# Kernel optimization log

Hardware: AMD Instinct MI355X
Metric: run time of the kernel (lower is better)

Reference implementation:

```python
import jax, jax.numpy as jnp
import numpy as np

B, L, DIN, DQ, DS, DP = 16, 2048, 1024, 128, 64, 32

def _lin(k, din, dout):
    k1, k2 = jax.random.split(k)
    s = 1.0 / np.sqrt(din)
    W = jax.random.uniform(k1, (din, dout), jnp.float32, -s, s)
    b = jax.random.uniform(k2, (dout,), jnp.float32, -s, s)
    return W, b

def setup_inputs() -> dict:
    key = jax.random.key(0)
    ks = jax.random.split(key, 13)
    Wq, bq = _lin(ks[0], DIN, DQ)
    Wk, bk = _lin(ks[1], DIN, DQ)
    Wv, bv = _lin(ks[2], DIN, DQ)
    W1, b1 = _lin(ks[3], DS + DP, 128)
    W2, b2 = _lin(ks[4], 128, DQ)
    Wqc, bqc = _lin(ks[5], DQ, DQ)
    Wkc, bkc = _lin(ks[6], DQ, DQ)
    return dict(
        query=jax.random.normal(ks[7], (B, L, DIN), jnp.float32),
        key=jax.random.normal(ks[8], (B, L, DIN), jnp.float32),
        value=jax.random.normal(ks[9], (B, L, DIN), jnp.float32),
        sf=jax.random.normal(ks[10], (B, DS), jnp.float32),
        pos=jax.random.normal(ks[11], (L, DP), jnp.float32),
        Wq=Wq, bq=bq, Wk=Wk, bk=bk, Wv=Wv, bv=bv,
        W1=W1, b1=b1, W2=W2, b2=b2,
        Wqc=Wqc, bqc=bqc, Wkc=Wkc, bkc=bkc,
    )

def reference(query, key, value, sf, pos,
              Wq, bq, Wk, bk, Wv, bv,
              W1, b1, W2, b2, Wqc, bqc, Wkc, bkc):
    b, l, _ = query.shape
    q = query @ Wq + bq            # [b, l, dq]
    k = key @ Wk + bk              # [b, l, dq]
    v = value @ Wv + bv            # [b, l, dq]
    # CPE bias branch (pos is not None)
    sf_exp = jnp.broadcast_to(sf[:, None, :], (b, l, sf.shape[1]))
    pos_exp = jnp.broadcast_to(pos[None, :, :], (b, l, pos.shape[1]))
    cpe = jnp.concatenate([sf_exp, pos_exp], axis=2)         # [b, l, ds+32]
    cpe = jax.nn.relu(cpe @ W1 + b1) @ W2 + b2               # [b, l, dq]
    qc = cpe @ Wqc + bqc
    kc = cpe @ Wkc + bkc
    bias = jnp.einsum('bld,bmd->blm', qc, kc)                # [b, l, l]
    # add_mode == 0: post-softmax additive bias
    scale = jnp.sqrt(jnp.asarray(q.shape[-1], q.dtype))
    scores = jnp.einsum('bld,bmd->blm', q, k) / scale
    attn = jax.nn.softmax(scores, axis=-1) + bias
    out = jnp.einsum('blm,bmd->bld', attn, v)
    # L1 diff-norm regularizer over bias (use_cls=False)
    norm3 = (jnp.sum(jnp.abs(bias[:, 1:, :] - bias[:, :-1, :])) +
             jnp.sum(jnp.abs(bias[:, :, 1:] - bias[:, :, :-1])))
    return out, norm3
```

## Files before the change

### kernel.cpp

```cpp
#include <hip/hip_runtime.h>
#include <hip/hip_bf16.h>

typedef __attribute__((ext_vector_type(8))) short short8;
typedef __attribute__((ext_vector_type(4))) short short4x;
typedef __attribute__((ext_vector_type(4))) float floatx4;

#define MFMA16(a,b,c) __builtin_amdgcn_mfma_f32_16x16x32_bf16((a),(b),(c),0,0,0)

__device__ __forceinline__ unsigned short f2bf(float f) {
  unsigned int x = __float_as_uint(f);
  return (unsigned short)((x + 0x7fffu + ((x >> 16) & 1u)) >> 16);
}
__device__ __forceinline__ float bf2f(unsigned short s) {
  return __uint_as_float(((unsigned int)s) << 16);
}
__device__ __forceinline__ unsigned short f2bf_cvt(float f) {
  unsigned int r;
  asm("v_cvt_pk_bf16_f32 %0, %1, %1" : "=v"(r) : "v"(f));
  return (unsigned short)r;
}
__device__ __forceinline__ short8 pack8(float4 f0, float4 f1) {
  union { unsigned int u[4]; short8 s; } r;
  asm("v_cvt_pk_bf16_f32 %0, %1, %2" : "=v"(r.u[0]) : "v"(f0.x), "v"(f0.y));
  asm("v_cvt_pk_bf16_f32 %0, %1, %2" : "=v"(r.u[1]) : "v"(f0.z), "v"(f0.w));
  asm("v_cvt_pk_bf16_f32 %0, %1, %2" : "=v"(r.u[2]) : "v"(f1.x), "v"(f1.y));
  asm("v_cvt_pk_bf16_f32 %0, %1, %2" : "=v"(r.u[3]) : "v"(f1.z), "v"(f1.w));
  return r.s;
}

typedef const __attribute__((address_space(1))) void* gas_ptr;
typedef __attribute__((address_space(3))) void* las_ptr;
__device__ __forceinline__ void gload_lds16(const void* g, void* s) {
  __builtin_amdgcn_global_load_lds((gas_ptr)g, (las_ptr)s, 16, 0, 0);
}

__global__ __launch_bounds__(256)
void prep_kernel(const float* __restrict__ Wq, const float* __restrict__ Wk,
                 const float* __restrict__ Wv, const float* __restrict__ W1,
                 const float* __restrict__ b1, const float* __restrict__ W2,
                 const float* __restrict__ b2, const float* __restrict__ Wqc,
                 const float* __restrict__ bqc, const float* __restrict__ Wkc,
                 const float* __restrict__ bkc, const float* __restrict__ sf,
                 const float* __restrict__ pos,
                 unsigned short* __restrict__ Wf, unsigned short* __restrict__ Ut,
                 float* __restrict__ cqck, float* __restrict__ Asf,
                 float* __restrict__ Ppos)
{
  int blk = blockIdx.x, t = threadIdx.x;
  if (blk < 24) {
    int mat = blk >> 3, cg = blk & 7;
    const float* W = (mat == 0) ? Wq : (mat == 1) ? Wk : Wv;
    int l = t & 63, jp = t >> 6;
    int col = cg * 16 + (l & 15);
    unsigned short* o = Wf + (size_t)mat * 131072 + (size_t)cg * 32 * 512 + l * 8 + jp * 2;
    for (int ks = 0; ks < 32; ++ks) {
      int k = ks * 32 + (l >> 4) * 8 + jp * 2;
      o[ks * 512 + 0] = f2bf(W[(size_t)k * 128 + col]);
      o[ks * 512 + 1] = f2bf(W[(size_t)(k + 1) * 128 + col]);
    }
  } else if (blk >= 384 && blk < 512) {
    int j = blk - 384;
    int k = t & 127;
    const float* Wc = (t < 128) ? Wqc : Wkc;
    float acc = 0.f;
    for (int h = 0; h < 128; ++h) acc += W2[k * 128 + h] * Wc[h * 128 + j];
    Ut[(size_t)((t < 128) ? j : 128 + j) * 128 + k] = f2bf(acc);
  } else if (blk == 512) {
    int j = t & 127;
    const float* Wc = (t < 128) ? Wqc : Wkc;
    const float* bc = (t < 128) ? bqc : bkc;
    float acc = bc[j];
    for (int k = 0; k < 128; ++k) acc += b2[k] * Wc[k * 128 + j];
    cqck[t] = acc;
  } else if (blk > 512 && blk < 529) {
    int b = blk - 513;
    if (t < 128) {
      float acc = 0.f;
      for (int i = 0; i < 64; ++i) acc += sf[b * 64 + i] * W1[i * 128 + t];
      Asf[b * 128 + t] = acc;
    }
  } else if (blk >= 529) {
    int l = blk - 529;
    if (t < 128) {
      float acc = b1[t];
      for (int i = 0; i < 32; ++i) acc += pos[l * 32 + i] * W1[(64 + i) * 128 + t];
      Ppos[l * 128 + t] = acc;
    }
  }
}

__global__ __launch_bounds__(256)
void proj_kernel(const float* __restrict__ X, const unsigned short* __restrict__ Wf,
                 const float* __restrict__ bias,
                 unsigned short* __restrict__ qo, unsigned short* __restrict__ ko,
                 unsigned short* __restrict__ vto, int which)
{
  __shared__ __align__(16) float X_lds[16 * 1028];

  int t = threadIdx.x, w = t >> 6, l = t & 63;
  int rowbase = blockIdx.x * 16;
  const int lrow = l & 15, hi = l >> 4;
  const float RS2 = 0.08838834764831845f * 1.4426950408889634f;

#pragma unroll
  for (int i = 0; i < 16; ++i) {
    int row = w * 4 + (i >> 2), seg = i & 3;
    gload_lds16(X + (size_t)(rowbase + row) * 1024 + seg * 256 + l * 4,
                (char*)X_lds + (size_t)row * 4112 + seg * 1024);
  }
  __syncthreads();

  const unsigned short* wp0 = Wf + (size_t)(w * 2) * 32 * 512 + l * 8;
  const unsigned short* wp1 = Wf + (size_t)(w * 2 + 1) * 32 * 512 + l * 8;
  const float* ap = &X_lds[lrow * 1028 + hi * 8];

  floatx4 acc0, acc1;
  acc0[0]=0.f; acc0[1]=0.f; acc0[2]=0.f; acc0[3]=0.f;
  acc1[0]=0.f; acc1[1]=0.f; acc1[2]=0.f; acc1[3]=0.f;

#pragma unroll 4
  for (int ks = 0; ks < 32; ++ks) {
    short8 b0 = *(const short8*)(wp0 + ks * 512);
    short8 b1 = *(const short8*)(wp1 + ks * 512);
    float4 f0 = *(const float4*)(ap + ks * 32);
    float4 f1 = *(const float4*)(ap + ks * 32 + 4);
    short8 a = pack8(f0, f1);
    acc0 = MFMA16(a, b0, acc0);
    acc1 = MFMA16(a, b1, acc1);
  }

#pragma unroll
  for (int nf = 0; nf < 2; ++nf) {
    int col = w * 32 + nf * 16 + lrow;
    float bb = bias[col];
    floatx4 av = (nf == 0) ? acc0 : acc1;
#pragma unroll
    for (int j = 0; j < 4; ++j) {
      int grow = rowbase + hi * 4 + j;
      float v = av[j] + bb;
      if (which == 0) qo[(size_t)grow * 128 + col] = f2bf(v * RS2);
      else if (which == 1) ko[(size_t)grow * 128 + col] = f2bf(v);
      else {
        int b = grow >> 11, li = grow & 2047;
        vto[((size_t)b * 128 + col) * 2048 + li] = f2bf(v);
      }
    }
  }
}

__global__ __launch_bounds__(256)
void qckc_kernel(const float* __restrict__ Asf, const float* __restrict__ Ppos,
                 const unsigned short* __restrict__ Ut, const float* __restrict__ cqck,
                 unsigned short* __restrict__ qc, unsigned short* __restrict__ kc)
{
  __shared__ __align__(16) unsigned short hid[64 * 136];
  int t = threadIdx.x, w = t >> 6, l = t & 63;
  int lbase = blockIdx.x * 64;
  int b = lbase >> 11;
  const int lrow = l & 15, lk = (l >> 4) * 8;
  {
    int r = t >> 2, seg = (t & 3) * 32;
    const float* pp = Ppos + (size_t)((lbase + r) & 2047) * 128 + seg;
    const float* aa = Asf + b * 128 + seg;
    unsigned short* dst = hid + r * 136 + seg;
#pragma unroll
    for (int c = 0; c < 32; c += 4) {
      float4 p4 = *(const float4*)(pp + c);
      float4 a4 = *(const float4*)(aa + c);
      dst[c + 0] = f2bf(fmaxf(p4.x + a4.x, 0.f));
      dst[c + 1] = f2bf(fmaxf(p4.y + a4.y, 0.f));
      dst[c + 2] = f2bf(fmaxf(p4.z + a4.z, 0.f));
      dst[c + 3] = f2bf(fmaxf(p4.w + a4.w, 0.f));
    }
  }
  __syncthreads();
  short8 a[4];
#pragma unroll
  for (int ks = 0; ks < 4; ++ks)
    a[ks] = *(const short8*)&hid[(w * 16 + lrow) * 136 + ks * 32 + lk];
  floatx4 acc[16];
#pragma unroll
  for (int nf = 0; nf < 16; ++nf) { acc[nf][0]=0.f; acc[nf][1]=0.f; acc[nf][2]=0.f; acc[nf][3]=0.f; }
#pragma unroll
  for (int nf = 0; nf < 16; ++nf)
#pragma unroll
    for (int ks = 0; ks < 4; ++ks) {
      short8 bfr = *(const short8*)(Ut + (size_t)(nf * 16 + lrow) * 128 + ks * 32 + lk);
      acc[nf] = MFMA16(a[ks], bfr, acc[nf]);
    }
#pragma unroll
  for (int nf = 0; nf < 16; ++nf) {
    int col = nf * 16 + lrow;
    float bb = cqck[col];
#pragma unroll
    for (int j = 0; j < 4; ++j) {
      int grow = lbase + w * 16 + (l >> 4) * 4 + j;
      float v = acc[nf][j] + bb;
      if (col < 128) qc[(size_t)grow * 128 + col] = f2bf(v);
      else kc[(size_t)grow * 128 + (col - 128)] = f2bf(v);
    }
  }
}

__global__ __launch_bounds__(256)
void m2_partial_kernel(const unsigned short* __restrict__ vt,
                       const unsigned short* __restrict__ kc,
                       float* __restrict__ M2p)
{
  __shared__ __align__(16) unsigned short kct[128 * 40];
  int ks = blockIdx.x, b = blockIdx.y;
  int t = threadIdx.x, w = t >> 6, l = t & 63;
  const int lrow = l & 15, lk = (l >> 4) * 8;
  floatx4 acc[2][8];
#pragma unroll
  for (int i = 0; i < 2; ++i)
#pragma unroll
    for (int j = 0; j < 8; ++j) { acc[i][j][0]=0.f; acc[i][j][1]=0.f; acc[i][j][2]=0.f; acc[i][j][3]=0.f; }
  for (int mc = 0; mc < 8; ++mc) {
    int mbase = ks * 256 + mc * 32;
    {
      int mm = t & 31, ib = (t >> 5) * 16;
      const unsigned short* src = kc + ((size_t)b * 2048 + mbase + mm) * 128 + ib;
#pragma unroll
      for (int ii = 0; ii < 16; ++ii) kct[(ib + ii) * 40 + mm] = src[ii];
    }
    __syncthreads();
#pragma unroll
    for (int mf = 0; mf < 2; ++mf) {
      int jrow = w * 32 + mf * 16 + lrow;
      short8 a = *(const short8*)(vt + ((size_t)b * 128 + jrow) * 2048 + mbase + lk);
#pragma unroll
      for (int nf = 0; nf < 8; ++nf) {
        short8 bfr = *(const short8*)&kct[(nf * 16 + lrow) * 40 + lk];
        acc[mf][nf] = MFMA16(a, bfr, acc[mf][nf]);
      }
    }
    __syncthreads();
  }
#pragma unroll
  for (int mf = 0; mf < 2; ++mf)
#pragma unroll
    for (int nf = 0; nf < 8; ++nf)
#pragma unroll
      for (int j = 0; j < 4; ++j) {
        int jr = w * 32 + mf * 16 + (l >> 4) * 4 + j;
        int ic = nf * 16 + lrow;
        M2p[(((size_t)ks * 16 + b) * 128 + jr) * 128 + ic] = acc[mf][nf][j];
      }
}

__global__ void m2_reduce_kernel(const float* __restrict__ M2p, float* __restrict__ M2t)
{
  int idx = blockIdx.x * 256 + threadIdx.x;
  float s = 0.f;
#pragma unroll
  for (int ksp = 0; ksp < 8; ++ksp) s += M2p[(size_t)ksp * 262144 + idx];
  M2t[idx] = s;
}

__global__ __launch_bounds__(256)
void attn_partial_kernel(const unsigned short* __restrict__ qbf,
                         const unsigned short* __restrict__ kbf,
                         const unsigned short* __restrict__ vt,
                         float* __restrict__ op, float* __restrict__ ms)
{
  __shared__ __align__(16) unsigned short K_lds[64 * 136];
  __shared__ __align__(16) unsigned short V_lds[128 * 72];
  __shared__ __align__(16) unsigned short P_lds[4 * 16 * 72];
  int t = threadIdx.x, w = t >> 6, l = t & 63;
  int lbase = blockIdx.x * 64, b = blockIdx.y, z = blockIdx.z;
  const int lrow = l & 15, lk = (l >> 4) * 8;

  size_t browq = (size_t)b * 2048 + lbase + w * 16 + lrow;
  short8 aq[4];
#pragma unroll
  for (int ks = 0; ks < 4; ++ks)
    aq[ks] = *(const short8*)(qbf + browq * 128 + ks * 32 + lk);

  float m_run[4] = {-1e30f, -1e30f, -1e30f, -1e30f};
  float s_run[4] = {0.f, 0.f, 0.f, 0.f};
  floatx4 o[8];
#pragma unroll
  for (int nf = 0; nf < 8; ++nf) { o[nf][0]=0.f; o[nf][1]=0.f; o[nf][2]=0.f; o[nf][3]=0.f; }

  int sr = t >> 2, sseg = (t & 3) * 32;
  int vr = t >> 1, vseg = (t & 1) * 32;

  const short8* ksrc0 = (const short8*)(kbf + ((size_t)b * 2048 + z * 1024 + sr) * 128 + sseg);
  const short8* vsrc0 = (const short8*)(vt + ((size_t)b * 128 + vr) * 2048 + z * 1024 + vseg);

  short8 kr[4], vrg[4];
#pragma unroll
  for (int i = 0; i < 4; ++i) { kr[i] = ksrc0[i]; vrg[i] = vsrc0[i]; }

  for (int kt = 0; kt < 16; ++kt) {
    {
      short8* dst = (short8*)&K_lds[sr * 136 + sseg];
      dst[0] = kr[0]; dst[1] = kr[1]; dst[2] = kr[2]; dst[3] = kr[3];
      short8* vdst = (short8*)&V_lds[vr * 72 + vseg];
      vdst[0] = vrg[0]; vdst[1] = vrg[1]; vdst[2] = vrg[2]; vdst[3] = vrg[3];
    }
    __syncthreads();
    if (kt < 15) {
      const short8* ks2 = ksrc0 + (size_t)(kt + 1) * 1024;
      const short8* vs2 = vsrc0 + (size_t)(kt + 1) * 8;
#pragma unroll
      for (int i = 0; i < 4; ++i) { kr[i] = ks2[i]; vrg[i] = vs2[i]; }
    }
    floatx4 s[4];
    __builtin_amdgcn_s_setprio(1);
#pragma unroll
    for (int cf = 0; cf < 4; ++cf) {
      floatx4 a4; a4[0]=0.f; a4[1]=0.f; a4[2]=0.f; a4[3]=0.f;
#pragma unroll
      for (int ks = 0; ks < 4; ++ks) {
        short8 bfr = *(const short8*)&K_lds[(cf * 16 + lrow) * 136 + ks * 32 + lk];
        a4 = MFMA16(aq[ks], bfr, a4);
      }
      s[cf] = a4;
    }
    __builtin_amdgcn_s_setprio(0);
    float tm[4];
#pragma unroll
    for (int j = 0; j < 4; ++j) {
      float m0 = fmaxf(fmaxf(s[0][j], s[1][j]), fmaxf(s[2][j], s[3][j]));
#pragma unroll
      for (int off = 1; off < 16; off <<= 1) m0 = fmaxf(m0, __shfl_xor(m0, off, 64));
      tm[j] = m0;
    }
    bool need = (tm[0] > m_run[0] + 8.f) | (tm[1] > m_run[1] + 8.f) |
                (tm[2] > m_run[2] + 8.f) | (tm[3] > m_run[3] + 8.f);
    if (__any(need)) {
      float fmul[4];
#pragma unroll
      for (int j = 0; j < 4; ++j) {
        float nm = fmaxf(m_run[j], tm[j]);
        fmul[j] = exp2f(m_run[j] - nm);
        m_run[j] = nm;
        s_run[j] *= fmul[j];
      }
#pragma unroll
      for (int nf = 0; nf < 8; ++nf)
#pragma unroll
        for (int j = 0; j < 4; ++j) o[nf][j] *= fmul[j];
    }
#pragma unroll
    for (int j = 0; j < 4; ++j) {
      float rs = 0.f;
#pragma unroll
      for (int cf = 0; cf < 4; ++cf) {
        float p = exp2f(s[cf][j] - m_run[j]);
        s[cf][j] = p;
        rs += p;
      }
#pragma unroll
      for (int off = 1; off < 16; off <<= 1) rs += __shfl_xor(rs, off, 64);
      s_run[j] += rs;
    }
    unsigned short* pw = P_lds + w * (16 * 72);
#pragma unroll
    for (int cf = 0; cf < 4; ++cf)
#pragma unroll
      for (int j = 0; j < 4; ++j)
        pw[((l >> 4) * 4 + j) * 72 + cf * 16 + lrow] = f2bf_cvt(s[cf][j]);
    __builtin_amdgcn_s_setprio(1);
#pragma unroll
    for (int kf = 0; kf < 2; ++kf) {
      short8 ap = *(const short8*)&pw[lrow * 72 + kf * 32 + lk];
#pragma unroll
      for (int nf = 0; nf < 8; ++nf) {
        short8 bv = *(const short8*)&V_lds[(nf * 16 + lrow) * 72 + kf * 32 + lk];
        o[nf] = MFMA16(ap, bv, o[nf]);
      }
    }
    __builtin_amdgcn_s_setprio(0);
    __syncthreads();
  }
  size_t obase = (size_t)(z * 16 + b) * 2048;
#pragma unroll
  for (int nf = 0; nf < 8; ++nf)
#pragma unroll
    for (int j = 0; j < 4; ++j) {
      int grow = lbase + w * 16 + (l >> 4) * 4 + j;
      op[(obase + grow) * 128 + nf * 16 + lrow] = o[nf][j];
    }
  if (lrow == 0) {
#pragma unroll
    for (int j = 0; j < 4; ++j) {
      int row = lbase + w * 16 + (l >> 4) * 4 + j;
      ms[(obase + row) * 2 + 0] = m_run[j];
      ms[(obase + row) * 2 + 1] = s_run[j];
    }
  }
}

__global__ __launch_bounds__(256)
void attn_merge_kernel(const float* __restrict__ op, const float* __restrict__ ms,
                       const unsigned short* __restrict__ qc,
                       const float* __restrict__ M2t, float* __restrict__ out)
{
  int t = threadIdx.x, w = t >> 6, l = t & 63;
  int lbase = blockIdx.x * 64, b = blockIdx.y;
  const int lrow = l & 15, lk = (l >> 4) * 8;
  size_t browq = (size_t)b * 2048 + lbase + w * 16 + lrow;

  float f0[4], f1[4], inv[4];
#pragma unroll
  for (int j = 0; j < 4; ++j) {
    int row = lbase + w * 16 + (l >> 4) * 4 + j;
    float m0 = ms[((size_t)(b) * 2048 + row) * 2 + 0];
    float s0 = ms[((size_t)(b) * 2048 + row) * 2 + 1];
    float m1 = ms[((size_t)(16 + b) * 2048 + row) * 2 + 0];
    float s1 = ms[((size_t)(16 + b) * 2048 + row) * 2 + 1];
    float M = fmaxf(m0, m1);
    f0[j] = exp2f(m0 - M);
    f1[j] = exp2f(m1 - M);
    inv[j] = 1.f / (s0 * f0[j] + s1 * f1[j]);
  }
  floatx4 o[8];
#pragma unroll
  for (int nf = 0; nf < 8; ++nf) {
    int col = nf * 16 + lrow;
#pragma unroll
    for (int j = 0; j < 4; ++j) {
      int grow = lbase + w * 16 + (l >> 4) * 4 + j;
      float o0 = op[((size_t)(b) * 2048 + grow) * 128 + col];
      float o1 = op[((size_t)(16 + b) * 2048 + grow) * 128 + col];
      o[nf][j] = (o0 * f0[j] + o1 * f1[j]) * inv[j];
    }
  }
#pragma unroll
  for (int ks = 0; ks < 4; ++ks) {
    short8 aqc = *(const short8*)(qc + browq * 128 + ks * 32 + lk);
#pragma unroll
    for (int nf = 0; nf < 8; ++nf) {
      const float* mp = M2t + ((size_t)b * 128 + nf * 16 + lrow) * 128 + ks * 32 + lk;
      float4 m0 = *(const float4*)(mp);
      float4 m1 = *(const float4*)(mp + 4);
      short8 bm = pack8(m0, m1);
      o[nf] = MFMA16(aqc, bm, o[nf]);
    }
  }
#pragma unroll
  for (int nf = 0; nf < 8; ++nf)
#pragma unroll
    for (int j = 0; j < 4; ++j) {
      int grow = lbase + w * 16 + (l >> 4) * 4 + j;
      out[((size_t)b * 2048 + grow) * 128 + nf * 16 + lrow] = o[nf][j];
    }
}

__global__ __launch_bounds__(256)
void norm_kernel(const unsigned short* __restrict__ qc, const unsigned short* __restrict__ kc,
                 float* __restrict__ partial)
{
  __shared__ __align__(16) unsigned short T1[129 * 136];
  __shared__ __align__(16) unsigned short T2[129 * 136];
  __shared__ float red[8];
  int t = threadIdx.x, w = t >> 6, l = t & 63;
  int ltm = blockIdx.x;
  int lt = ltm >> 4, mt = ltm & 15;
  int b = blockIdx.y;
  const int lrow = l & 15, lk = (l >> 4) * 8;
  {
    int r = t >> 1, half = (t & 1) * 64;
    const unsigned short* asrc = qc + ((size_t)b * 2048 + lt * 128 + r) * 128 + half;
    const unsigned short* bsrc = kc + ((size_t)b * 2048 + mt * 128 + r) * 128 + half;
    unsigned short* adst = T1 + r * 136 + half;
    unsigned short* bdst = T2 + r * 136 + half;
#pragma unroll
    for (int c = 0; c < 64; c += 8) {
      *(short8*)(adst + c) = *(const short8*)(asrc + c);
      *(short8*)(bdst + c) = *(const short8*)(bsrc + c);
    }
    if (t < 16) {
      int gr = lt * 128 + 128; if (gr > 2047) gr = 2047;
      *(short8*)(T1 + 128 * 136 + t * 8) =
          *(const short8*)(qc + ((size_t)b * 2048 + gr) * 128 + t * 8);
    } else if (t < 32) {
      int c = (t - 16) * 8;
      int gr = mt * 128 + 128; if (gr > 2047) gr = 2047;
      *(short8*)(T2 + 128 * 136 + c) =
          *(const short8*)(kc + ((size_t)b * 2048 + gr) * 128 + c);
    }
  }
  __syncthreads();
  floatx4 acc0[2][8], acc1[2][8];
#pragma unroll
  for (int i = 0; i < 2; ++i)
#pragma unroll
    for (int j = 0; j < 8; ++j) {
      acc0[i][j][0]=0.f; acc0[i][j][1]=0.f; acc0[i][j][2]=0.f; acc0[i][j][3]=0.f;
      acc1[i][j][0]=0.f; acc1[i][j][1]=0.f; acc1[i][j][2]=0.f; acc1[i][j][3]=0.f;
    }
#pragma unroll
  for (int ks = 0; ks < 4; ++ks) {
    int off = ks * 32 + lk;
    short8 ad[2], cd[2];
#pragma unroll
    for (int mf = 0; mf < 2; ++mf) {
      int r = w * 32 + mf * 16 + lrow;
      short8 x1 = *(const short8*)&T1[r * 136 + off];
      short8 y1 = *(const short8*)&T1[(r + 1) * 136 + off];
      short8 x2 = *(const short8*)&T2[r * 136 + off];
      short8 y2 = *(const short8*)&T2[(r + 1) * 136 + off];
      short8 d1, d2;
#pragma unroll
      for (int ii = 0; ii < 8; ++ii) {
        d1[ii] = (short)f2bf(bf2f((unsigned short)y1[ii]) - bf2f((unsigned short)x1[ii]));
        d2[ii] = (short)f2bf(bf2f((unsigned short)y2[ii]) - bf2f((unsigned short)x2[ii]));
      }
      ad[mf] = d1; cd[mf] = d2;
    }
#pragma unroll
    for (int nf = 0; nf < 8; ++nf) {
      short8 bk = *(const short8*)&T2[(nf * 16 + lrow) * 136 + off];
      short8 bq = *(const short8*)&T1[(nf * 16 + lrow) * 136 + off];
      acc0[0][nf] = MFMA16(ad[0], bk, acc0[0][nf]);
      acc0[1][nf] = MFMA16(ad[1], bk, acc0[1][nf]);
      acc1[0][nf] = MFMA16(cd[0], bq, acc1[0][nf]);
      acc1[1][nf] = MFMA16(cd[1], bq, acc1[1][nf]);
    }
  }
  float s0 = 0.f, s1 = 0.f;
#pragma unroll
  for (int i = 0; i < 2; ++i)
#pragma unroll
    for (int nf = 0; nf < 8; ++nf)
#pragma unroll
      for (int j = 0; j < 4; ++j) {
        s0 += fabsf(acc0[i][nf][j]);
        s1 += fabsf(acc1[i][nf][j]);
      }
#pragma unroll
  for (int off = 1; off < 64; off <<= 1) {
    s0 += __shfl_xor(s0, off, 64);
    s1 += __shfl_xor(s1, off, 64);
  }
  if (l == 0) { red[w] = s0; red[4 + w] = s1; }
  __syncthreads();
  if (t == 0) {
    partial[((size_t)0 * 16 + b) * 256 + ltm] = red[0] + red[1] + red[2] + red[3];
    partial[((size_t)1 * 16 + b) * 256 + ltm] = red[4] + red[5] + red[6] + red[7];
  }
}

__global__ void norm_reduce_kernel(const float* __restrict__ partial, float* __restrict__ outp)
{
  __shared__ float red[4];
  int t = threadIdx.x;
  float s = 0.f;
  for (int i = t; i < 8192; i += 256) s += partial[i];
#pragma unroll
  for (int off = 1; off < 64; off <<= 1) s += __shfl_xor(s, off, 64);
  if ((t & 63) == 0) red[t >> 6] = s;
  __syncthreads();
  if (t == 0) outp[0] = red[0] + red[1] + red[2] + red[3];
}

extern "C" void kernel_launch(void* const* d_in, const int* in_sizes, int n_in,
                              void* d_out, int out_size, void* d_ws, size_t ws_size,
                              hipStream_t stream)
{
  const float* query = (const float*)d_in[0];
  const float* key_  = (const float*)d_in[1];
  const float* value = (const float*)d_in[2];
  const float* sf    = (const float*)d_in[3];
  const float* pos   = (const float*)d_in[4];
  const float* Wq  = (const float*)d_in[5];  const float* bq  = (const float*)d_in[6];
  const float* Wk  = (const float*)d_in[7];  const float* bk  = (const float*)d_in[8];
  const float* Wv  = (const float*)d_in[9];  const float* bv  = (const float*)d_in[10];
  const float* W1  = (const float*)d_in[11]; const float* b1  = (const float*)d_in[12];
  const float* W2  = (const float*)d_in[13]; const float* b2  = (const float*)d_in[14];
  const float* Wqc = (const float*)d_in[15]; const float* bqc = (const float*)d_in[16];
  const float* Wkc = (const float*)d_in[17]; const float* bkc = (const float*)d_in[18];
  float* out = (float*)d_out;

  char* ws = (char*)d_ws;
  size_t off = 0;
  auto alloc = [&](size_t bytes) {
    char* p = ws + off;
    off += (bytes + 255) & ~(size_t)255;
    return p;
  };
  unsigned short* Wf   = (unsigned short*)alloc((size_t)3 * 131072 * 2);
  unsigned short* Ut   = (unsigned short*)alloc((size_t)256 * 128 * 2);
  float* cqck          = (float*)alloc(256 * 4);
  float* Asf           = (float*)alloc(16 * 128 * 4);
  float* Ppos          = (float*)alloc((size_t)2048 * 128 * 4);
  unsigned short* qbf  = (unsigned short*)alloc((size_t)32768 * 128 * 2);
  unsigned short* kbf  = (unsigned short*)alloc((size_t)32768 * 128 * 2);
  unsigned short* vt   = (unsigned short*)alloc((size_t)32768 * 128 * 2);
  unsigned short* qc   = (unsigned short*)alloc((size_t)32768 * 128 * 2);
  unsigned short* kc   = (unsigned short*)alloc((size_t)32768 * 128 * 2);
  float* M2p           = (float*)alloc((size_t)8 * 262144 * 4);
  float* M2t           = (float*)alloc((size_t)262144 * 4);
  float* npartial      = (float*)alloc((size_t)8192 * 4);
  float* op            = (float*)alloc((size_t)32 * 2048 * 128 * 4);
  float* ms            = (float*)alloc((size_t)32 * 2048 * 2 * 4);
  (void)ws_size; (void)in_sizes; (void)n_in; (void)out_size;

  prep_kernel<<<2577, 256, 0, stream>>>(Wq, Wk, Wv, W1, b1, W2, b2, Wqc, bqc, Wkc, bkc,
                                        sf, pos, Wf, Ut, cqck, Asf, Ppos);
  proj_kernel<<<2048, 256, 0, stream>>>(query, Wf,          bq, qbf, kbf, vt, 0);
  proj_kernel<<<2048, 256, 0, stream>>>(key_,  Wf + 131072, bk, qbf, kbf, vt, 1);
  proj_kernel<<<2048, 256, 0, stream>>>(value, Wf + 262144, bv, qbf, kbf, vt, 2);
  qckc_kernel<<<512, 256, 0, stream>>>(Asf, Ppos, Ut, cqck, qc, kc);
  m2_partial_kernel<<<dim3(8, 16), 256, 0, stream>>>(vt, kc, M2p);
  m2_reduce_kernel<<<1024, 256, 0, stream>>>(M2p, M2t);
  attn_partial_kernel<<<dim3(32, 16, 2), 256, 0, stream>>>(qbf, kbf, vt, op, ms);
  attn_merge_kernel<<<dim3(32, 16), 256, 0, stream>>>(op, ms, qc, M2t, out);
  norm_kernel<<<dim3(256, 16), 256, 0, stream>>>(qc, kc, npartial);
  norm_reduce_kernel<<<1, 256, 0, stream>>>(npartial, out + (size_t)4194304);
}
```

Baseline: 371.0 us.

## Stage bf16 X tiles with 32-row blocks in projection; load V fragments directly

The projection kernel now converts X to bf16 while loading it through registers into LDS, rather than using an async fp32 global-to-LDS copy. Each block covers 32 rows instead of 16, so every weight fragment read from global memory feeds twice as many MFMAs, and half as many blocks are launched. The attention kernel drops the V LDS staging and loads V fragments straight from global memory into registers each tile. This removes LDS traffic for V and the fp32 X footprint, at the cost of more register pressure, uncoalesced strided V loads and the loss of async copies in the projection.

```diff
diff --git a/kernel.cpp b/kernel.cpp
--- a/kernel.cpp
+++ b/kernel.cpp
@@ -26,12 +26,6 @@
   asm("v_cvt_pk_bf16_f32 %0, %1, %2" : "=v"(r.u[2]) : "v"(f1.x), "v"(f1.y));
   asm("v_cvt_pk_bf16_f32 %0, %1, %2" : "=v"(r.u[3]) : "v"(f1.z), "v"(f1.w));
   return r.s;
-}
-
-typedef const __attribute__((address_space(1))) void* gas_ptr;
-typedef __attribute__((address_space(3))) void* las_ptr;
-__device__ __forceinline__ void gload_lds16(const void* g, void* s) {
-  __builtin_amdgcn_global_load_lds((gas_ptr)g, (las_ptr)s, 16, 0, 0);
 }
 
 __global__ __launch_bounds__(256)
@@ -95,57 +89,70 @@
                  unsigned short* __restrict__ qo, unsigned short* __restrict__ ko,
                  unsigned short* __restrict__ vto, int which)
 {
-  __shared__ __align__(16) float X_lds[16 * 1028];
+  __shared__ __align__(16) unsigned short X_lds[32 * 1032];
 
   int t = threadIdx.x, w = t >> 6, l = t & 63;
-  int rowbase = blockIdx.x * 16;
+  int rowbase = blockIdx.x * 32;
   const int lrow = l & 15, hi = l >> 4;
   const float RS2 = 0.08838834764831845f * 1.4426950408889634f;
 
 #pragma unroll
-  for (int i = 0; i < 16; ++i) {
-    int row = w * 4 + (i >> 2), seg = i & 3;
-    gload_lds16(X + (size_t)(rowbase + row) * 1024 + seg * 256 + l * 4,
-                (char*)X_lds + (size_t)row * 4112 + seg * 1024);
+  for (int r = 0; r < 8; ++r) {
+    int row = w * 8 + r;
+    const float* src = X + (size_t)(rowbase + row) * 1024 + l * 4;
+    unsigned short* dst = &X_lds[row * 1032 + l * 4];
+#pragma unroll
+    for (int i = 0; i < 4; ++i) {
+      float4 v = *(const float4*)(src + i * 256);
+      short4x s;
+      s[0] = (short)f2bf(v.x); s[1] = (short)f2bf(v.y);
+      s[2] = (short)f2bf(v.z); s[3] = (short)f2bf(v.w);
+      *(short4x*)(dst + i * 256) = s;
+    }
   }
   __syncthreads();
 
   const unsigned short* wp0 = Wf + (size_t)(w * 2) * 32 * 512 + l * 8;
   const unsigned short* wp1 = Wf + (size_t)(w * 2 + 1) * 32 * 512 + l * 8;
-  const float* ap = &X_lds[lrow * 1028 + hi * 8];
-
-  floatx4 acc0, acc1;
-  acc0[0]=0.f; acc0[1]=0.f; acc0[2]=0.f; acc0[3]=0.f;
-  acc1[0]=0.f; acc1[1]=0.f; acc1[2]=0.f; acc1[3]=0.f;
+  const int xo0 = lrow * 1032 + hi * 8;
+  const int xo1 = (lrow + 16) * 1032 + hi * 8;
+
+  floatx4 acc[2][2];
+#pragma unroll
+  for (int i = 0; i < 2; ++i)
+#pragma unroll
+    for (int j = 0; j < 2; ++j) { acc[i][j][0]=0.f; acc[i][j][1]=0.f; acc[i][j][2]=0.f; acc[i][j][3]=0.f; }
 
 #pragma unroll 4
   for (int ks = 0; ks < 32; ++ks) {
     short8 b0 = *(const short8*)(wp0 + ks * 512);
     short8 b1 = *(const short8*)(wp1 + ks * 512);
-    float4 f0 = *(const float4*)(ap + ks * 32);
-    float4 f1 = *(const float4*)(ap + ks * 32 + 4);
-    short8 a = pack8(f0, f1);
-    acc0 = MFMA16(a, b0, acc0);
-    acc1 = MFMA16(a, b1, acc1);
-  }
-
-#pragma unroll
-  for (int nf = 0; nf < 2; ++nf) {
-    int col = w * 32 + nf * 16 + lrow;
-    float bb = bias[col];
-    floatx4 av = (nf == 0) ? acc0 : acc1;
-#pragma unroll
-    for (int j = 0; j < 4; ++j) {
-      int grow = rowbase + hi * 4 + j;
-      float v = av[j] + bb;
-      if (which == 0) qo[(size_t)grow * 128 + col] = f2bf(v * RS2);
-      else if (which == 1) ko[(size_t)grow * 128 + col] = f2bf(v);
-      else {
-        int b = grow >> 11, li = grow & 2047;
-        vto[((size_t)b * 128 + col) * 2048 + li] = f2bf(v);
-      }
-    }
-  }
+    short8 a0 = *(const short8*)&X_lds[xo0 + ks * 32];
+    short8 a1 = *(const short8*)&X_lds[xo1 + ks * 32];
+    acc[0][0] = MFMA16(a0, b0, acc[0][0]);
+    acc[0][1] = MFMA16(a0, b1, acc[0][1]);
+    acc[1][0] = MFMA16(a1, b0, acc[1][0]);
+    acc[1][1] = MFMA16(a1, b1, acc[1][1]);
+  }
+
+#pragma unroll
+  for (int mf = 0; mf < 2; ++mf)
+#pragma unroll
+    for (int nf = 0; nf < 2; ++nf) {
+      int col = w * 32 + nf * 16 + lrow;
+      float bb = bias[col];
+#pragma unroll
+      for (int j = 0; j < 4; ++j) {
+        int grow = rowbase + mf * 16 + hi * 4 + j;
+        float v = acc[mf][nf][j] + bb;
+        if (which == 0) qo[(size_t)grow * 128 + col] = f2bf(v * RS2);
+        else if (which == 1) ko[(size_t)grow * 128 + col] = f2bf(v);
+        else {
+          int b = grow >> 11, li = grow & 2047;
+          vto[((size_t)b * 128 + col) * 2048 + li] = f2bf(v);
+        }
+      }
+    }
 }
 
 __global__ __launch_bounds__(256)
@@ -265,7 +272,6 @@
                          float* __restrict__ op, float* __restrict__ ms)
 {
   __shared__ __align__(16) unsigned short K_lds[64 * 136];
-  __shared__ __align__(16) unsigned short V_lds[128 * 72];
   __shared__ __align__(16) unsigned short P_lds[4 * 16 * 72];
   int t = threadIdx.x, w = t >> 6, l = t & 63;
   int lbase = blockIdx.x * 64, b = blockIdx.y, z = blockIdx.z;
@@ -284,29 +290,31 @@
   for (int nf = 0; nf < 8; ++nf) { o[nf][0]=0.f; o[nf][1]=0.f; o[nf][2]=0.f; o[nf][3]=0.f; }
 
   int sr = t >> 2, sseg = (t & 3) * 32;
-  int vr = t >> 1, vseg = (t & 1) * 32;
 
   const short8* ksrc0 = (const short8*)(kbf + ((size_t)b * 2048 + z * 1024 + sr) * 128 + sseg);
-  const short8* vsrc0 = (const short8*)(vt + ((size_t)b * 128 + vr) * 2048 + z * 1024 + vseg);
-
-  short8 kr[4], vrg[4];
-#pragma unroll
-  for (int i = 0; i < 4; ++i) { kr[i] = ksrc0[i]; vrg[i] = vsrc0[i]; }
+  const unsigned short* vfb = vt + ((size_t)b * 128 + lrow) * 2048 + z * 1024 + lk;
+
+  short8 kr[4];
+#pragma unroll
+  for (int i = 0; i < 4; ++i) kr[i] = ksrc0[i];
 
   for (int kt = 0; kt < 16; ++kt) {
     {
       short8* dst = (short8*)&K_lds[sr * 136 + sseg];
       dst[0] = kr[0]; dst[1] = kr[1]; dst[2] = kr[2]; dst[3] = kr[3];
-      short8* vdst = (short8*)&V_lds[vr * 72 + vseg];
-      vdst[0] = vrg[0]; vdst[1] = vrg[1]; vdst[2] = vrg[2]; vdst[3] = vrg[3];
     }
     __syncthreads();
     if (kt < 15) {
       const short8* ks2 = ksrc0 + (size_t)(kt + 1) * 1024;
-      const short8* vs2 = vsrc0 + (size_t)(kt + 1) * 8;
-#pragma unroll
-      for (int i = 0; i < 4; ++i) { kr[i] = ks2[i]; vrg[i] = vs2[i]; }
-    }
+#pragma unroll
+      for (int i = 0; i < 4; ++i) kr[i] = ks2[i];
+    }
+    short8 vb[8][2];
+#pragma unroll
+    for (int nf = 0; nf < 8; ++nf)
+#pragma unroll
+      for (int kf = 0; kf < 2; ++kf)
+        vb[nf][kf] = *(const short8*)(vfb + (size_t)(nf * 16) * 2048 + kt * 64 + kf * 32);
     floatx4 s[4];
     __builtin_amdgcn_s_setprio(1);
 #pragma unroll
@@ -368,10 +376,8 @@
     for (int kf = 0; kf < 2; ++kf) {
       short8 ap = *(const short8*)&pw[lrow * 72 + kf * 32 + lk];
 #pragma unroll
-      for (int nf = 0; nf < 8; ++nf) {
-        short8 bv = *(const short8*)&V_lds[(nf * 16 + lrow) * 72 + kf * 32 + lk];
-        o[nf] = MFMA16(ap, bv, o[nf]);
-      }
+      for (int nf = 0; nf < 8; ++nf)
+        o[nf] = MFMA16(ap, vb[nf][kf], o[nf]);
     }
     __builtin_amdgcn_s_setprio(0);
     __syncthreads();
@@ -602,9 +608,9 @@
 
   prep_kernel<<<2577, 256, 0, stream>>>(Wq, Wk, Wv, W1, b1, W2, b2, Wqc, bqc, Wkc, bkc,
                                         sf, pos, Wf, Ut, cqck, Asf, Ppos);
-  proj_kernel<<<2048, 256, 0, stream>>>(query, Wf,          bq, qbf, kbf, vt, 0);
-  proj_kernel<<<2048, 256, 0, stream>>>(key_,  Wf + 131072, bk, qbf, kbf, vt, 1);
-  proj_kernel<<<2048, 256, 0, stream>>>(value, Wf + 262144, bv, qbf, kbf, vt, 2);
+  proj_kernel<<<1024, 256, 0, stream>>>(query, Wf,          bq, qbf, kbf, vt, 0);
+  proj_kernel<<<1024, 256, 0, stream>>>(key_,  Wf + 131072, bk, qbf, kbf, vt, 1);
+  proj_kernel<<<1024, 256, 0, stream>>>(value, Wf + 262144, bv, qbf, kbf, vt, 2);
   qckc_kernel<<<512, 256, 0, stream>>>(Asf, Ppos, Ut, cqck, qc, kc);
   m2_partial_kernel<<<dim3(8, 16), 256, 0, stream>>>(vt, kc, M2p);
   m2_reduce_kernel<<<1024, 256, 0, stream>>>(M2p, M2t);
```

After: 421.9 us. 13.7% more time.
